# Performance work log

Measured on AMD Instinct MI355X. Metric: run time of the kernel, lower is better.

## Reference

```python
import jax, jax.numpy as jnp
import numpy as np

N_AGENTS = 64
_adj = np.ones((N_AGENTS, N_AGENTS)) - np.eye(N_AGENTS)
SEND_NP, RECV_NP = np.where(_adj)  # 4032 directed edges, no self-loops
N_EDGES = SEND_NP.shape[0]

D_NODE = 16
H = 64
D_OUT = 16
N_TYPES = 2
BATCH = 128


def _glorot(key, shape):
    fan_in, fan_out = shape[0], shape[1]
    lim = np.sqrt(6.0 / (fan_in + fan_out)).astype(np.float32)
    return jax.random.uniform(key, shape, jnp.float32, -lim, lim)


def setup_inputs() -> dict:
    key = jax.random.key(0)
    ks = jax.random.split(key, 16)
    inp = {
        "node_states": jax.random.normal(ks[0], (BATCH, N_AGENTS, 1, D_NODE), jnp.float32),
        "edge_types": jax.random.uniform(ks[1], (BATCH, N_EDGES, N_TYPES + 1, 1), jnp.float32),
        # edge encoder 0: MLP(32 -> 64 -> 64)
        "e0_w1": _glorot(ks[2], (2 * D_NODE, H)), "e0_b1": jnp.zeros((H,), jnp.float32),
        "e0_w2": _glorot(ks[3], (H, H)), "e0_b2": jnp.zeros((H,), jnp.float32),
        # edge encoder 1
        "e1_w1": _glorot(ks[4], (2 * D_NODE, H)), "e1_b1": jnp.zeros((H,), jnp.float32),
        "e1_w2": _glorot(ks[5], (H, H)), "e1_b2": jnp.zeros((H,), jnp.float32),
        # node decoder: MLP(16+64 -> 64 -> 16)
        "nd_w1": _glorot(ks[6], (D_NODE + H, H)), "nd_b1": jnp.zeros((H,), jnp.float32),
        "nd_w2": _glorot(ks[7], (H, D_OUT)), "nd_b2": jnp.zeros((D_OUT,), jnp.float32),
    }
    return inp


def _mlp2(x, w1, b1, w2, b2):
    h = jax.nn.relu(x @ w1 + b1)
    return jax.nn.relu(h @ w2 + b2)


def reference(node_states, edge_types,
              e0_w1, e0_b1, e0_w2, e0_b2,
              e1_w1, e1_b1, e1_w2, e1_b2,
              nd_w1, nd_b1, nd_w2, nd_b2):
    send = jnp.asarray(SEND_NP)
    recv = jnp.asarray(RECV_NP)
    # NodeAggregator: gather sender/receiver states to edges -> [B, E, 1, 2D]
    edge_msg = jnp.concatenate([node_states[:, send], node_states[:, recv]], axis=-1)
    # per-edge-type MLP encode, concat along axis 2 -> [B, E, T, H]
    enc0 = _mlp2(edge_msg, e0_w1, e0_b1, e0_w2, e0_b2)
    enc1 = _mlp2(edge_msg, e1_w1, e1_b1, e1_w2, e1_b2)
    encoded = jnp.concatenate([enc0, enc1], axis=2)
    # masked sum over edge types (skip type-0 'no edge') -> [B, E, 1, H]
    edge_msg_sum = jnp.sum(encoded * edge_types[:, :, 1:, :], axis=2, keepdims=True)
    # EdgeAggregator: scatter-sum edge messages to receiver nodes -> [B, N, 1, H]
    node_msg = jax.ops.segment_sum(
        edge_msg_sum.swapaxes(0, 1), recv, num_segments=N_AGENTS).swapaxes(0, 1)
    # decode
    node_state = jnp.concatenate([node_states, node_msg], axis=-1)  # [B, N, 1, D+H]
    return _mlp2(node_state, nd_w1, nd_b1, nd_w2, nd_b2)
```

## Files before the change

kernel.cpp:

```cpp
#include <hip/hip_runtime.h>
#include <hip/hip_bf16.h>


typedef __attribute__((ext_vector_type(8))) short bh8;
typedef __attribute__((ext_vector_type(4))) float fv4;

union AB { bh8 v; __hip_bfloat162 h[4]; };

__global__ __launch_bounds__(256) void fused_kernel(
    const float* __restrict__ ns, const float* __restrict__ et,
    const float* __restrict__ e0w1, const float* __restrict__ e0b1,
    const float* __restrict__ e0w2, const float* __restrict__ e0b2,
    const float* __restrict__ e1w1, const float* __restrict__ e1b1,
    const float* __restrict__ e1w2, const float* __restrict__ e1b2,
    const float* __restrict__ ndw1, const float* __restrict__ ndb1,
    const float* __restrict__ ndw2, const float* __restrict__ ndb2,
    float* __restrict__ out)
{
  __shared__ float NSl[64*16];
  __shared__ float Pl[2*64*68];
  __shared__ float Qb[2*8*64];
  __shared__ float ETl[2*8*64];
  __shared__ float MSG[8*64];

  int t = threadIdx.x;
  int b = blockIdx.x >> 3, rg = blockIdx.x & 7, r0 = rg*8;
  int w = t >> 6, lane = t & 63, quad = lane >> 4, col = lane & 15;

  ((float4*)NSl)[t] = ((const float4*)(ns + b*1024))[t];
  __syncthreads();

  {
    int h = lane;
#pragma unroll
    for (int enc = 0; enc < 2; ++enc) {
      const float* w1 = enc ? e1w1 : e0w1;
      float wc[16];
#pragma unroll
      for (int k = 0; k < 16; ++k) wc[k] = w1[k*64 + h];
      float* pdst = Pl + enc*4352;
#pragma unroll
      for (int si = 0; si < 16; ++si) {
        int s = w*16 + si;
        const float* x = NSl + s*16;
        float acc = 0.f;
#pragma unroll
        for (int k = 0; k < 16; ++k) acc += wc[k] * x[k];
        pdst[s*68 + h] = acc;
      }
    }
  }
#pragma unroll
  for (int i = 0; i < 4; ++i) {
    int idx = i*256 + t;
    int enc = idx >> 9, rem = idx & 511;
    int rl = rem >> 6, h = rem & 63;
    const float* w1 = enc ? e1w1 : e0w1;
    const float* b1 = enc ? e1b1 : e0b1;
    const float* x = NSl + (r0 + rl)*16;
    float acc = b1[h];
#pragma unroll
    for (int k = 0; k < 16; ++k) acc += w1[(16 + k)*64 + h] * x[k];
    Qb[idx] = acc;
  }
#pragma unroll
  for (int i = 0; i < 2; ++i) {
    int idx = i*256 + t;
    int s = idx >> 3, rl = idx & 7;
    int r = r0 + rl;
    float v0 = 0.f, v1 = 0.f;
    if (s != r) {
      int pos = r - (r > s ? 1 : 0);
      const float* base = et + (b*4032 + s*63 + pos)*3;
      v0 = base[1]; v1 = base[2];
    }
    ETl[rl*64 + s] = v0;
    ETl[512 + rl*64 + s] = v1;
  }
  __syncthreads();

  float msgacc[2][4] = {{0.f,0.f,0.f,0.f},{0.f,0.f,0.f,0.f}};

#pragma unroll
  for (int enc = 0; enc < 2; ++enc) {
    const float* w2 = enc ? e1w2 : e0w2;
    const float* b2 = enc ? e1b2 : e0b2;
    bh8 bf[4][2];
    float b2v[4];
#pragma unroll
    for (int nt = 0; nt < 4; ++nt) {
#pragma unroll
      for (int kk = 0; kk < 2; ++kk) {
        const float* base = w2 + (kk*32 + quad*8)*64 + nt*16 + col;
        float f0 = base[0*64], f1 = base[1*64], f2 = base[2*64], f3 = base[3*64];
        float f4 = base[4*64], f5 = base[5*64], f6 = base[6*64], f7 = base[7*64];
        AB bb;
        bb.h[0] = __float22bfloat162_rn(make_float2(f0, f1));
        bb.h[1] = __float22bfloat162_rn(make_float2(f2, f3));
        bb.h[2] = __float22bfloat162_rn(make_float2(f4, f5));
        bb.h[3] = __float22bfloat162_rn(make_float2(f6, f7));
        bf[nt][kk] = bb.v;
      }
      b2v[nt] = b2[nt*16 + col];
    }
#pragma unroll
    for (int rli = 0; rli < 2; ++rli) {
      int rl = w*2 + rli;
      const float* qrow = Qb + (enc*8 + rl)*64;
      float4 qa0 = *(const float4*)(qrow + quad*8);
      float4 qa1 = *(const float4*)(qrow + quad*8 + 4);
      float4 qb0 = *(const float4*)(qrow + 32 + quad*8);
      float4 qb1 = *(const float4*)(qrow + 32 + quad*8 + 4);
      const float* etrow = ETl + (enc*8 + rl)*64;
#pragma unroll
      for (int st = 0; st < 4; ++st) {
        const float* prow = Pl + enc*4352 + (st*16 + col)*68;
        float4 pa0 = *(const float4*)(prow + quad*8);
        float4 pa1 = *(const float4*)(prow + quad*8 + 4);
        float4 pb0 = *(const float4*)(prow + 32 + quad*8);
        float4 pb1 = *(const float4*)(prow + 32 + quad*8 + 4);
        AB a0, a1;
        a0.h[0] = __float22bfloat162_rn(make_float2(fmaxf(pa0.x + qa0.x, 0.f), fmaxf(pa0.y + qa0.y, 0.f)));
        a0.h[1] = __float22bfloat162_rn(make_float2(fmaxf(pa0.z + qa0.z, 0.f), fmaxf(pa0.w + qa0.w, 0.f)));
        a0.h[2] = __float22bfloat162_rn(make_float2(fmaxf(pa1.x + qa1.x, 0.f), fmaxf(pa1.y + qa1.y, 0.f)));
        a0.h[3] = __float22bfloat162_rn(make_float2(fmaxf(pa1.z + qa1.z, 0.f), fmaxf(pa1.w + qa1.w, 0.f)));
        a1.h[0] = __float22bfloat162_rn(make_float2(fmaxf(pb0.x + qb0.x, 0.f), fmaxf(pb0.y + qb0.y, 0.f)));
        a1.h[1] = __float22bfloat162_rn(make_float2(fmaxf(pb0.z + qb0.z, 0.f), fmaxf(pb0.w + qb0.w, 0.f)));
        a1.h[2] = __float22bfloat162_rn(make_float2(fmaxf(pb1.x + qb1.x, 0.f), fmaxf(pb1.y + qb1.y, 0.f)));
        a1.h[3] = __float22bfloat162_rn(make_float2(fmaxf(pb1.z + qb1.z, 0.f), fmaxf(pb1.w + qb1.w, 0.f)));
        float4 etv = *(const float4*)(etrow + st*16 + quad*4);
#pragma unroll
        for (int nt = 0; nt < 4; ++nt) {
          fv4 acc = {b2v[nt], b2v[nt], b2v[nt], b2v[nt]};
          acc = __builtin_amdgcn_mfma_f32_16x16x32_bf16(a0.v, bf[nt][0], acc, 0, 0, 0);
          acc = __builtin_amdgcn_mfma_f32_16x16x32_bf16(a1.v, bf[nt][1], acc, 0, 0, 0);
          float m = msgacc[rli][nt];
          m += etv.x * fmaxf(acc[0], 0.f);
          m += etv.y * fmaxf(acc[1], 0.f);
          m += etv.z * fmaxf(acc[2], 0.f);
          m += etv.w * fmaxf(acc[3], 0.f);
          msgacc[rli][nt] = m;
        }
      }
    }
  }
#pragma unroll
  for (int rli = 0; rli < 2; ++rli) {
#pragma unroll
    for (int nt = 0; nt < 4; ++nt) {
      float v = msgacc[rli][nt];
      v += __shfl_xor(v, 16);
      v += __shfl_xor(v, 32);
      if (lane < 16) MSG[(w*2 + rli)*64 + nt*16 + lane] = v;
    }
  }
  __syncthreads();

  float* HD = Pl;
#pragma unroll
  for (int pass = 0; pass < 2; ++pass) {
    int idx = pass*256 + t;
    int rl = idx >> 6, j = idx & 63;
    float acc = ndb1[j];
    const float* x0 = NSl + (r0 + rl)*16;
#pragma unroll
    for (int i = 0; i < 16; ++i) acc += x0[i] * ndw1[i*64 + j];
    const float* mrow = MSG + rl*64;
#pragma unroll
    for (int i = 0; i < 64; ++i) acc += mrow[i] * ndw1[(16 + i)*64 + j];
    HD[idx] = fmaxf(acc, 0.f);
  }
  __syncthreads();
  if (t < 128) {
    int rl = t >> 4, o = t & 15;
    float acc = ndb2[o];
#pragma unroll
    for (int j = 0; j < 64; ++j) acc += HD[rl*64 + j] * ndw2[j*16 + o];
    out[(b*64 + r0 + rl)*16 + o] = fmaxf(acc, 0.f);
  }
}

extern "C" void kernel_launch(void* const* d_in, const int* in_sizes, int n_in,
                              void* d_out, int out_size, void* d_ws, size_t ws_size,
                              hipStream_t stream) {
  const float* ns   = (const float*)d_in[0];
  const float* et   = (const float*)d_in[1];
  const float* e0w1 = (const float*)d_in[2];
  const float* e0b1 = (const float*)d_in[3];
  const float* e0w2 = (const float*)d_in[4];
  const float* e0b2 = (const float*)d_in[5];
  const float* e1w1 = (const float*)d_in[6];
  const float* e1b1 = (const float*)d_in[7];
  const float* e1w2 = (const float*)d_in[8];
  const float* e1b2 = (const float*)d_in[9];
  const float* ndw1 = (const float*)d_in[10];
  const float* ndb1 = (const float*)d_in[11];
  const float* ndw2 = (const float*)d_in[12];
  const float* ndb2 = (const float*)d_in[13];

  fused_kernel<<<1024, 256, 0, stream>>>(ns, et,
                                         e0w1, e0b1, e0w2, e0b2,
                                         e1w1, e1b1, e1w2, e1b2,
                                         ndw1, ndb1, ndw2, ndb2,
                                         (float*)d_out);
}
```

Measured before the change: 133.4 us.

## Compute sender projections with MFMA, store in bf16 LDS, and constrain unrolling

The per-sender first-layer projection (16 to 64) now runs on MFMA bf16 instructions, with the K dimension zero-padded from 16 to 32, instead of scalar FMAs. The results go to LDS as bf16, which halves the shared memory footprint and the LDS read traffic in the edge loop. Launch bounds now ask for 4 blocks per SM, and the unroll pragmas are reduced to cut register pressure. Storing the projection in bf16 adds a rounding step before the bias add and ReLU, and the zero-padded MFMA wastes half its K lanes.

```diff
diff --git a/kernel.cpp b/kernel.cpp
--- a/kernel.cpp
+++ b/kernel.cpp
@@ -7,7 +7,7 @@
 
 union AB { bh8 v; __hip_bfloat162 h[4]; };
 
-__global__ __launch_bounds__(256) void fused_kernel(
+__global__ __launch_bounds__(256, 4) void fused_kernel(
     const float* __restrict__ ns, const float* __restrict__ et,
     const float* __restrict__ e0w1, const float* __restrict__ e0b1,
     const float* __restrict__ e0w2, const float* __restrict__ e0b2,
@@ -18,7 +18,7 @@
     float* __restrict__ out)
 {
   __shared__ float NSl[64*16];
-  __shared__ float Pl[2*64*68];
+  __shared__ __align__(16) __hip_bfloat16 Plh[2*64*72];
   __shared__ float Qb[2*8*64];
   __shared__ float ETl[2*8*64];
   __shared__ float MSG[8*64];
@@ -30,23 +30,44 @@
   ((float4*)NSl)[t] = ((const float4*)(ns + b*1024))[t];
   __syncthreads();
 
+  const __hip_bfloat162 zz = __float22bfloat162_rn(make_float2(0.f, 0.f));
+
   {
-    int h = lane;
-#pragma unroll
+    AB a;
+    if (quad < 2) {
+      const float* xr = NSl + (w*16 + col)*16 + quad*8;
+      float4 x0 = *(const float4*)xr;
+      float4 x1 = *(const float4*)(xr + 4);
+      a.h[0] = __float22bfloat162_rn(make_float2(x0.x, x0.y));
+      a.h[1] = __float22bfloat162_rn(make_float2(x0.z, x0.w));
+      a.h[2] = __float22bfloat162_rn(make_float2(x1.x, x1.y));
+      a.h[3] = __float22bfloat162_rn(make_float2(x1.z, x1.w));
+    } else {
+      a.h[0] = a.h[1] = a.h[2] = a.h[3] = zz;
+    }
+#pragma unroll 1
     for (int enc = 0; enc < 2; ++enc) {
       const float* w1 = enc ? e1w1 : e0w1;
-      float wc[16];
-#pragma unroll
-      for (int k = 0; k < 16; ++k) wc[k] = w1[k*64 + h];
-      float* pdst = Pl + enc*4352;
-#pragma unroll
-      for (int si = 0; si < 16; ++si) {
-        int s = w*16 + si;
-        const float* x = NSl + s*16;
-        float acc = 0.f;
-#pragma unroll
-        for (int k = 0; k < 16; ++k) acc += wc[k] * x[k];
-        pdst[s*68 + h] = acc;
+#pragma unroll
+      for (int ht = 0; ht < 4; ++ht) {
+        AB bb;
+        if (quad < 2) {
+#pragma unroll
+          for (int j = 0; j < 4; ++j) {
+            float f0 = w1[(quad*8 + 2*j    )*64 + ht*16 + col];
+            float f1 = w1[(quad*8 + 2*j + 1)*64 + ht*16 + col];
+            bb.h[j] = __float22bfloat162_rn(make_float2(f0, f1));
+          }
+        } else {
+          bb.h[0] = bb.h[1] = bb.h[2] = bb.h[3] = zz;
+        }
+        fv4 acc = {0.f, 0.f, 0.f, 0.f};
+        acc = __builtin_amdgcn_mfma_f32_16x16x32_bf16(a.v, bb.v, acc, 0, 0, 0);
+        __hip_bfloat16* pd = Plh + enc*4608 + (w*16 + quad*4)*72 + ht*16 + col;
+        pd[0*72] = __float2bfloat16(acc[0]);
+        pd[1*72] = __float2bfloat16(acc[1]);
+        pd[2*72] = __float2bfloat16(acc[2]);
+        pd[3*72] = __float2bfloat16(acc[3]);
       }
     }
   }
@@ -81,7 +102,7 @@
 
   float msgacc[2][4] = {{0.f,0.f,0.f,0.f},{0.f,0.f,0.f,0.f}};
 
-#pragma unroll
+#pragma unroll 1
   for (int enc = 0; enc < 2; ++enc) {
     const float* w2 = enc ? e1w2 : e0w2;
     const float* b2 = enc ? e1b2 : e0b2;
@@ -92,18 +113,16 @@
 #pragma unroll
       for (int kk = 0; kk < 2; ++kk) {
         const float* base = w2 + (kk*32 + quad*8)*64 + nt*16 + col;
-        float f0 = base[0*64], f1 = base[1*64], f2 = base[2*64], f3 = base[3*64];
-        float f4 = base[4*64], f5 = base[5*64], f6 = base[6*64], f7 = base[7*64];
         AB bb;
-        bb.h[0] = __float22bfloat162_rn(make_float2(f0, f1));
-        bb.h[1] = __float22bfloat162_rn(make_float2(f2, f3));
-        bb.h[2] = __float22bfloat162_rn(make_float2(f4, f5));
-        bb.h[3] = __float22bfloat162_rn(make_float2(f6, f7));
+        bb.h[0] = __float22bfloat162_rn(make_float2(base[0*64], base[1*64]));
+        bb.h[1] = __float22bfloat162_rn(make_float2(base[2*64], base[3*64]));
+        bb.h[2] = __float22bfloat162_rn(make_float2(base[4*64], base[5*64]));
+        bb.h[3] = __float22bfloat162_rn(make_float2(base[6*64], base[7*64]));
         bf[nt][kk] = bb.v;
       }
       b2v[nt] = b2[nt*16 + col];
     }
-#pragma unroll
+#pragma unroll 1
     for (int rli = 0; rli < 2; ++rli) {
       int rl = w*2 + rli;
       const float* qrow = Qb + (enc*8 + rl)*64;
@@ -112,22 +131,31 @@
       float4 qb0 = *(const float4*)(qrow + 32 + quad*8);
       float4 qb1 = *(const float4*)(qrow + 32 + quad*8 + 4);
       const float* etrow = ETl + (enc*8 + rl)*64;
-#pragma unroll
+#pragma unroll 2
       for (int st = 0; st < 4; ++st) {
-        const float* prow = Pl + enc*4352 + (st*16 + col)*68;
-        float4 pa0 = *(const float4*)(prow + quad*8);
-        float4 pa1 = *(const float4*)(prow + quad*8 + 4);
-        float4 pb0 = *(const float4*)(prow + 32 + quad*8);
-        float4 pb1 = *(const float4*)(prow + 32 + quad*8 + 4);
+        const __hip_bfloat16* prow = Plh + enc*4608 + (st*16 + col)*72 + quad*8;
+        AB p0, p1;
+        p0.v = *(const bh8*)prow;
+        p1.v = *(const bh8*)(prow + 32);
         AB a0, a1;
-        a0.h[0] = __float22bfloat162_rn(make_float2(fmaxf(pa0.x + qa0.x, 0.f), fmaxf(pa0.y + qa0.y, 0.f)));
-        a0.h[1] = __float22bfloat162_rn(make_float2(fmaxf(pa0.z + qa0.z, 0.f), fmaxf(pa0.w + qa0.w, 0.f)));
-        a0.h[2] = __float22bfloat162_rn(make_float2(fmaxf(pa1.x + qa1.x, 0.f), fmaxf(pa1.y + qa1.y, 0.f)));
-        a0.h[3] = __float22bfloat162_rn(make_float2(fmaxf(pa1.z + qa1.z, 0.f), fmaxf(pa1.w + qa1.w, 0.f)));
-        a1.h[0] = __float22bfloat162_rn(make_float2(fmaxf(pb0.x + qb0.x, 0.f), fmaxf(pb0.y + qb0.y, 0.f)));
-        a1.h[1] = __float22bfloat162_rn(make_float2(fmaxf(pb0.z + qb0.z, 0.f), fmaxf(pb0.w + qb0.w, 0.f)));
-        a1.h[2] = __float22bfloat162_rn(make_float2(fmaxf(pb1.x + qb1.x, 0.f), fmaxf(pb1.y + qb1.y, 0.f)));
-        a1.h[3] = __float22bfloat162_rn(make_float2(fmaxf(pb1.z + qb1.z, 0.f), fmaxf(pb1.w + qb1.w, 0.f)));
+        {
+          float2 f0 = __bfloat1622float2(p0.h[0]);
+          float2 f1 = __bfloat1622float2(p0.h[1]);
+          float2 f2 = __bfloat1622float2(p0.h[2]);
+          float2 f3 = __bfloat1622float2(p0.h[3]);
+          a0.h[0] = __float22bfloat162_rn(make_float2(fmaxf(f0.x + qa0.x, 0.f), fmaxf(f0.y + qa0.y, 0.f)));
+          a0.h[1] = __float22bfloat162_rn(make_float2(fmaxf(f1.x + qa0.z, 0.f), fmaxf(f1.y + qa0.w, 0.f)));
+          a0.h[2] = __float22bfloat162_rn(make_float2(fmaxf(f2.x + qa1.x, 0.f), fmaxf(f2.y + qa1.y, 0.f)));
+          a0.h[3] = __float22bfloat162_rn(make_float2(fmaxf(f3.x + qa1.z, 0.f), fmaxf(f3.y + qa1.w, 0.f)));
+          float2 g0 = __bfloat1622float2(p1.h[0]);
+          float2 g1 = __bfloat1622float2(p1.h[1]);
+          float2 g2 = __bfloat1622float2(p1.h[2]);
+          float2 g3 = __bfloat1622float2(p1.h[3]);
+          a1.h[0] = __float22bfloat162_rn(make_float2(fmaxf(g0.x + qb0.x, 0.f), fmaxf(g0.y + qb0.y, 0.f)));
+          a1.h[1] = __float22bfloat162_rn(make_float2(fmaxf(g1.x + qb0.z, 0.f), fmaxf(g1.y + qb0.w, 0.f)));
+          a1.h[2] = __float22bfloat162_rn(make_float2(fmaxf(g2.x + qb1.x, 0.f), fmaxf(g2.y + qb1.y, 0.f)));
+          a1.h[3] = __float22bfloat162_rn(make_float2(fmaxf(g3.x + qb1.z, 0.f), fmaxf(g3.y + qb1.w, 0.f)));
+        }
         float4 etv = *(const float4*)(etrow + st*16 + quad*4);
 #pragma unroll
         for (int nt = 0; nt < 4; ++nt) {
@@ -156,7 +184,7 @@
   }
   __syncthreads();
 
-  float* HD = Pl;
+  float* HD = (float*)Plh;
 #pragma unroll
   for (int pass = 0; pass < 2; ++pass) {
     int idx = pass*256 + t;
```

New measurement: 112.3 us. -15.8%, faster.
